# Kernel tuning notes

Measured on AMD Instinct MI355X. Metric: run time of the kernel, lower is better.

Reference implementation:

```python
import jax, jax.numpy as jnp
import numpy as np
from jax import lax

DIM = 512
HEADS = 8
B, H, W = 8, 64, 64
EPS = 1e-12  # F.normalize default eps


def pointwise(x, w):
    # 1x1 conv, no bias: [B,C,H,W] x [O,C] -> [B,O,H,W]
    return jnp.einsum('oc,bchw->bohw', w, x)


def depthwise3x3(x, dw):
    # groups=C depthwise 3x3 conv, padding=1, no bias. dw: [C,1,3,3]
    return lax.conv_general_dilated(
        x, dw, window_strides=(1, 1), padding=((1, 1), (1, 1)),
        feature_group_count=x.shape[1],
        dimension_numbers=('NCHW', 'OIHW', 'NCHW'))


def setup_inputs() -> dict:
    key = jax.random.key(0)
    ks = jax.random.split(key, 8)
    s = 1.0 / np.sqrt(DIM)
    return {
        'x': jax.random.normal(ks[0], (B, DIM, H, W), jnp.float32),
        'w_q': jax.random.normal(ks[1], (DIM, DIM), jnp.float32) * s,
        'w_k': jax.random.normal(ks[2], (DIM, DIM), jnp.float32) * s,
        'w_v': jax.random.normal(ks[3], (DIM, DIM), jnp.float32) * s,
        'dw_q': jax.random.normal(ks[4], (DIM, 1, 3, 3), jnp.float32) * (1.0 / 3.0),
        'dw_k': jax.random.normal(ks[5], (DIM, 1, 3, 3), jnp.float32) * (1.0 / 3.0),
        'dw_v': jax.random.normal(ks[6], (DIM, 1, 3, 3), jnp.float32) * (1.0 / 3.0),
        'w_proj': jax.random.normal(ks[7], (DIM, DIM), jnp.float32) * s,
        'temperature': jnp.ones((HEADS, 1, 1), jnp.float32),
    }


def reference(x, w_q, w_k, w_v, dw_q, dw_k, dw_v, w_proj, temperature):
    b, c, h, w = x.shape
    d = c // HEADS
    hw = h * w

    q = depthwise3x3(pointwise(x, w_q), dw_q)
    k = depthwise3x3(pointwise(x, w_k), dw_k)
    v = depthwise3x3(pointwise(x, w_v), dw_v)

    # b (h d) x y -> b h d (x y)
    q = q.reshape(b, HEADS, d, hw)
    k = k.reshape(b, HEADS, d, hw)
    v = v.reshape(b, HEADS, d, hw)

    # L2-normalize over spatial axis (F.normalize, eps=1e-12)
    q = q / jnp.maximum(jnp.linalg.norm(q, axis=-1, keepdims=True), EPS)
    k = k / jnp.maximum(jnp.linalg.norm(k, axis=-1, keepdims=True), EPS)

    # channel attention: [b,h,d,d]
    attn = jnp.einsum('bhdn,bhen->bhde', q, k) * temperature
    attn = jax.nn.softmax(attn, axis=-1)
    out = jnp.einsum('bhde,bhen->bhdn', attn, v)  # [b,h,d,hw]

    out = out.reshape(b, c, h, w)
    return pointwise(out, w_proj)
```

## Files before the change

### kernel.cpp

```cpp
#include <hip/hip_runtime.h>
#include <hip/hip_bf16.h>
#include <stdint.h>

#define DEV __device__ __forceinline__

typedef __attribute__((ext_vector_type(8))) short   s16x8;
typedef __attribute__((ext_vector_type(8))) __bf16  bf16x8;
typedef __attribute__((ext_vector_type(4))) float   f32x4;

static constexpr int BATCH = 8;
static constexpr int DIM   = 512;
static constexpr int HEADS = 8;
static constexpr int HD    = 64;
static constexpr int HW    = 4096;
static constexpr int CQKV  = 1536;
static constexpr int NSPLIT = 8;

DEV void gload16(const void* g, void* l) {
  __builtin_amdgcn_global_load_lds(
      (const __attribute__((address_space(1))) void*)g,
      (__attribute__((address_space(3))) void*)l,
      16, 0, 0);
}

DEV f32x4 mfma16x32(s16x8 a, s16x8 b, f32x4 c) {
  return __builtin_amdgcn_mfma_f32_16x16x32_bf16(
      __builtin_bit_cast(bf16x8, a), __builtin_bit_cast(bf16x8, b), c, 0, 0, 0);
}

DEV float b2f(short x) {
  unsigned u = (unsigned)(unsigned short)x << 16;
  return __uint_as_float(u);
}
DEV short f2b(float f) { return __builtin_bit_cast(short, __float2bfloat16(f)); }

__global__ __launch_bounds__(256) void prep_weights(
    const float* __restrict__ wq, const float* __restrict__ wk,
    const float* __restrict__ wv, const float* __restrict__ wp,
    __hip_bfloat16* __restrict__ wqkv, __hip_bfloat16* __restrict__ wpb)
{
  int i = blockIdx.x * 256 + threadIdx.x;
  if (i < CQKV * DIM) {
    int r = i / DIM;
    const float* src = (r < 512) ? wq : (r < 1024) ? wk : wv;
    wqkv[i] = __float2bfloat16(src[(r & 511) * DIM + (i % DIM)]);
  } else {
    int j = i - CQKV * DIM;
    wpb[j] = __float2bfloat16(wp[j]);
  }
}

__global__ __launch_bounds__(256) void transpose_x(
    const float* __restrict__ x, __hip_bfloat16* __restrict__ XT)
{
  __shared__ float tile[64 * 65];
  const int n0 = blockIdx.x * 64, c0 = blockIdx.y * 64, b = blockIdx.z;
  const int t = threadIdx.x;
#pragma unroll
  for (int i = 0; i < 16; ++i) {
    int f = i * 256 + t; int ci = f >> 6, nj = f & 63;
    tile[ci * 65 + nj] = x[((long)b * DIM + c0 + ci) * HW + n0 + nj];
  }
  __syncthreads();
#pragma unroll
  for (int i = 0; i < 16; ++i) {
    int f = i * 256 + t; int ni = f >> 6, cj = f & 63;
    XT[((long)b * HW + n0 + ni) * DIM + c0 + cj] = __float2bfloat16(tile[cj * 65 + ni]);
  }
}

__global__ __launch_bounds__(256) void gemm_bt(
    const __hip_bfloat16* __restrict__ A,
    const __hip_bfloat16* __restrict__ Bt,
    __hip_bfloat16* __restrict__ Cout,
    int M, int N, int K, long bt_bstride, long c_bstride)
{
  __shared__ __hip_bfloat16 lds[16896];
  const int t = threadIdx.x, w = t >> 6, l = t & 63;
  const int m0 = blockIdx.y * 128, n0 = blockIdx.x * 128, b = blockIdx.z;
  const int wr = w >> 1, wc = w & 1;
  const __hip_bfloat16* Bb = Bt + (long)b * bt_bstride;
  __hip_bfloat16* ldsA = lds;
  __hip_bfloat16* ldsB = lds + 8192;

  f32x4 acc[4][4] = {};

  for (int k0 = 0; k0 < K; k0 += 64) {
#pragma unroll
    for (int i = 0; i < 4; ++i) {
      int r = w * 32 + i * 8 + (l >> 3);
      int c = (l & 7) ^ (r & 7);
      gload16(A  + (long)(m0 + r) * K + k0 + c * 8, &ldsA[w * 2048 + i * 512]);
      gload16(Bb + (long)(n0 + r) * K + k0 + c * 8, &ldsB[w * 2048 + i * 512]);
    }
    __syncthreads();
#pragma unroll
    for (int kk = 0; kk < 64; kk += 32) {
      s16x8 af[4], bfr[4];
#pragma unroll
      for (int mi = 0; mi < 4; ++mi) {
        int ar = wr * 64 + mi * 16 + (l & 15);
        int col = (kk + (l >> 4) * 8) ^ ((ar & 7) << 3);
        af[mi] = *(const s16x8*)&ldsA[ar * 64 + col];
      }
#pragma unroll
      for (int ni = 0; ni < 4; ++ni) {
        int br = wc * 64 + ni * 16 + (l & 15);
        int col = (kk + (l >> 4) * 8) ^ ((br & 7) << 3);
        bfr[ni] = *(const s16x8*)&ldsB[br * 64 + col];
      }
#pragma unroll
      for (int mi = 0; mi < 4; ++mi)
#pragma unroll
        for (int ni = 0; ni < 4; ++ni)
          acc[mi][ni] = mfma16x32(af[mi], bfr[ni], acc[mi][ni]);
    }
    __syncthreads();
  }

#pragma unroll
  for (int mi = 0; mi < 4; ++mi)
#pragma unroll
    for (int ni = 0; ni < 4; ++ni)
#pragma unroll
      for (int j = 0; j < 4; ++j) {
        int r = wr * 64 + mi * 16 + (l >> 4) * 4 + j;
        int c = wc * 64 + ni * 16 + (l & 15);
        lds[r * 132 + c] = __float2bfloat16(acc[mi][ni][j]);
      }
  __syncthreads();
  __hip_bfloat16* crow = Cout + (long)b * c_bstride + (long)m0 * N + n0;
#pragma unroll
  for (int q = 0; q < 8; ++q) {
    int chunk = q * 256 + t;
    int r = chunk >> 4, c = (chunk & 15) * 8;
    s16x8 v = *(const s16x8*)&lds[r * 132 + c];
    *(s16x8*)&crow[(long)r * N + c] = v;
  }
}

template <bool OUT_BF16>
__global__ __launch_bounds__(512, 2) void gemm_bt8(
    const __hip_bfloat16* __restrict__ A,
    const __hip_bfloat16* __restrict__ Bt,
    void* __restrict__ Cout,
    int M, int N, int K, long bt_bstride, long c_bstride)
{
  __shared__ __hip_bfloat16 lds[65536];
  const int t = threadIdx.x, w = t >> 6, l = t & 63;
  const int wm = w >> 2, wn = w & 3;
  const int m0 = blockIdx.y * 256, n0 = blockIdx.x * 256, b = blockIdx.z;
  const __hip_bfloat16* Bb = Bt + (long)b * bt_bstride;

  const int rl = t >> 3;
  const int ch = ((t & 7) ^ (rl & 7)) * 8;
  const int fr = l & 15, fk = (l >> 4) * 8;
  const int fswz = (l & 7) << 3;

  auto stageA = [&](int p, int h, int u) {
    const __hip_bfloat16* src = A + (long)(m0 + h * 64 + rl) * K + u * 64 + ch;
    __hip_bfloat16* dst = lds + p * 16384 + h * 8192 + w * 512;
    gload16(src, dst);
    gload16(src + 128l * K, dst + 4096);
  };
  auto stageB = [&](int p, int hb, int u) {
    const __hip_bfloat16* src = Bb + (long)(n0 + hb * 128 + rl) * K + u * 64 + ch;
    __hip_bfloat16* dst = lds + 32768 + p * 16384 + hb * 8192 + w * 512;
    gload16(src, dst);
    gload16(src + 64l * K, dst + 4096);
  };

  f32x4 acc[8][4] = {};
  const int NT = K >> 6;

  stageB(0, 0, 0); stageB(0, 1, 0); stageA(0, 0, 0); stageA(0, 1, 0);
  stageB(1, 0, 1); stageB(1, 1, 1); stageA(1, 0, 1);
  asm volatile("s_waitcnt vmcnt(6)" ::: "memory");
  __builtin_amdgcn_s_barrier();

  for (int u = 0; u < NT; ++u) {
    const int p = u & 1;
    const __hip_bfloat16* lA = lds + p * 16384 + wm * 4096;
    const __hip_bfloat16* lB = lds + 32768 + p * 16384 + (wn >> 1) * 8192
                             + (wn & 1) * 4096;
    s16x8 bfr[2][4];
#pragma unroll
    for (int q = 0; q < 4; ++q) {
      s16x8 afr[2][2];
#pragma unroll
      for (int kk = 0; kk < 2; ++kk)
#pragma unroll
        for (int mi = 0; mi < 2; ++mi)
          afr[kk][mi] = *(const s16x8*)&lA[(q >> 1) * 8192
              + ((q & 1) * 32 + mi * 16 + fr) * 64 + ((kk * 32 + fk) ^ fswz)];
      if (q == 0) {
#pragma unroll
        for (int kk = 0; kk < 2; ++kk)
#pragma unroll
          for (int ni = 0; ni < 4; ++ni)
            bfr[kk][ni] = *(const s16x8*)&lB[(ni * 16 + fr) * 64
                + ((kk * 32 + fk) ^ fswz)];
      }
      if (q == 0)      { if (u + 1 < NT) stageA(p ^ 1, 1, u + 1); }
      else if (q == 1) { if (u + 2 < NT) stageB(p, 0, u + 2); }
      else if (q == 2) { if (u + 2 < NT) stageB(p, 1, u + 2); }
      else {
        if (u + 2 < NT) stageA(p, 0, u + 2);
        if (u == NT - 2) asm volatile("s_waitcnt vmcnt(0)" ::: "memory");
        else             asm volatile("s_waitcnt vmcnt(6)" ::: "memory");
      }
      __builtin_amdgcn_s_barrier();
      asm volatile("s_waitcnt lgkmcnt(0)" ::: "memory");
      __builtin_amdgcn_sched_barrier(0);
      __builtin_amdgcn_s_setprio(1);
#pragma unroll
      for (int kk = 0; kk < 2; ++kk)
#pragma unroll
        for (int mi = 0; mi < 2; ++mi)
#pragma unroll
          for (int ni = 0; ni < 4; ++ni)
            acc[q * 2 + mi][ni] = mfma16x32(afr[kk][mi], bfr[kk][ni],
                                            acc[q * 2 + mi][ni]);
      __builtin_amdgcn_s_setprio(0);
      __builtin_amdgcn_s_barrier();
    }
  }

  const int row0 = m0 + wm * 128, col0 = n0 + wn * 64;
#pragma unroll
  for (int mi = 0; mi < 8; ++mi)
#pragma unroll
    for (int ni = 0; ni < 4; ++ni)
#pragma unroll
      for (int j = 0; j < 4; ++j) {
        long rr = row0 + mi * 16 + (l >> 4) * 4 + j;
        long cc = col0 + ni * 16 + fr;
        float v = acc[mi][ni][j];
        if (OUT_BF16)
          ((__hip_bfloat16*)Cout)[(long)b * c_bstride + rr * N + cc] = __float2bfloat16(v);
        else
          ((float*)Cout)[(long)b * c_bstride + rr * N + cc] = v;
      }
}

__global__ __launch_bounds__(256) void dwconv(
    __hip_bfloat16* __restrict__ P,
    const float* __restrict__ dwq, const float* __restrict__ dwk,
    const float* __restrict__ dwv, float* __restrict__ rnorm)
{
  __shared__ float pl[66 * 67];
  __shared__ float red4[4];
  const int c = blockIdx.x, b = blockIdx.y, t = threadIdx.x;
  const int w = t >> 6, l = t & 63;

  if (t < 66) { pl[t] = 0.f; pl[65 * 67 + t] = 0.f; }
  if (t >= 128 && t < 192) { pl[(t - 127) * 67] = 0.f; }
  if (t >= 192)            { pl[(t - 191) * 67 + 65] = 0.f; }

  const long base = ((long)b * CQKV + c) * HW;
  const int y = t >> 2, x0 = (t & 3) * 16;
  s16x8 v0 = *(const s16x8*)&P[base + t * 16];
  s16x8 v1 = *(const s16x8*)&P[base + t * 16 + 8];
#pragma unroll
  for (int j = 0; j < 8; ++j) {
    pl[(y + 1) * 67 + x0 + 1 + j] = b2f(v0[j]);
    pl[(y + 1) * 67 + x0 + 9 + j] = b2f(v1[j]);
  }
  __syncthreads();

  const int qkv = c >> 9, cc = c & 511;
  const float* dw = ((qkv == 0) ? dwq : (qkv == 1) ? dwk : dwv) + (long)cc * 9;
  const float w0 = dw[0], w1 = dw[1], w2 = dw[2], w3 = dw[3], w4 = dw[4],
              w5 = dw[5], w6 = dw[6], w7 = dw[7], w8 = dw[8];

  const float* r0 = &pl[y * 67 + x0];
  float outv[16];
  float ss = 0.f;
#pragma unroll
  for (int j = 0; j < 16; ++j) {
    float s = w0 * r0[j]       + w1 * r0[j + 1]   + w2 * r0[j + 2]
            + w3 * r0[j + 67]  + w4 * r0[j + 68]  + w5 * r0[j + 69]
            + w6 * r0[j + 134] + w7 * r0[j + 135] + w8 * r0[j + 136];
    outv[j] = s;
    ss += s * s;
  }
  s16x8 o0, o1;
#pragma unroll
  for (int j = 0; j < 8; ++j) { o0[j] = f2b(outv[j]); o1[j] = f2b(outv[j + 8]); }
  *(s16x8*)&P[base + t * 16]     = o0;
  *(s16x8*)&P[base + t * 16 + 8] = o1;

  if (qkv < 2) {
#pragma unroll
    for (int off = 32; off; off >>= 1) ss += __shfl_down(ss, off);
    if (l == 0) red4[w] = ss;
    __syncthreads();
    if (t == 0)
      rnorm[(long)b * 1024 + qkv * 512 + cc] =
          1.f / fmaxf(sqrtf(red4[0] + red4[1] + red4[2] + red4[3]), 1e-12f);
  }
}

__global__ __launch_bounds__(256) void transpose_v(
    const __hip_bfloat16* __restrict__ P, __hip_bfloat16* __restrict__ VT)
{
  __shared__ __hip_bfloat16 tile[64 * 65];
  const int n0 = blockIdx.x * 64, h = blockIdx.y, b = blockIdx.z;
  const int t = threadIdx.x;
#pragma unroll
  for (int i = 0; i < 16; ++i) {
    int f = i * 256 + t; int ei = f >> 6, nj = f & 63;
    tile[ei * 65 + nj] = P[((long)b * CQKV + 1024 + h * HD + ei) * HW + n0 + nj];
  }
  __syncthreads();
#pragma unroll
  for (int i = 0; i < 16; ++i) {
    int f = i * 256 + t; int ni = f >> 6, ej = f & 63;
    VT[(((long)b * HEADS + h) * HW + n0 + ni) * HD + ej] = tile[ej * 65 + ni];
  }
}

__global__ __launch_bounds__(256) void attn_partial(__hip_bfloat16* __restrict__ P)
{
  __shared__ __hip_bfloat16 ldsQ[64 * 128];
  __shared__ __hip_bfloat16 ldsK[64 * 128];
  const int t = threadIdx.x, w = t >> 6, l = t & 63;
  const int sp = blockIdx.x, h = blockIdx.y, b = blockIdx.z;
  const int wr = w >> 1, wc = w & 1;

  const long qbase = ((long)b * CQKV + h * HD) * HW;
  const long kbase = ((long)b * CQKV + 512 + h * HD) * HW;

  f32x4 acc[2][2] = {};

  const int kend = sp * 512 + 512;
  for (int k0 = sp * 512; k0 < kend; k0 += 128) {
#pragma unroll
    for (int i = 0; i < 4; ++i) {
      int r = w * 16 + i * 4 + (l >> 4);
      int c = (l & 15) ^ (r & 7);
      gload16(P + qbase + (long)r * HW + k0 + c * 8, &ldsQ[w * 2048 + i * 512]);
      gload16(P + kbase + (long)r * HW + k0 + c * 8, &ldsK[w * 2048 + i * 512]);
    }
    __syncthreads();
#pragma unroll
    for (int kk = 0; kk < 128; kk += 32) {
      s16x8 af[2], bfr[2];
#pragma unroll
      for (int mi = 0; mi < 2; ++mi) {
        int ar = wr * 32 + mi * 16 + (l & 15);
        int col = (kk + (l >> 4) * 8) ^ ((ar & 7) << 3);
        af[mi] = *(const s16x8*)&ldsQ[ar * 128 + col];
      }
#pragma unroll
      for (int ni = 0; ni < 2; ++ni) {
        int br = wc * 32 + ni * 16 + (l & 15);
        int col = (kk + (l >> 4) * 8) ^ ((br & 7) << 3);
        bfr[ni] = *(const s16x8*)&ldsK[br * 128 + col];
      }
#pragma unroll
      for (int mi = 0; mi < 2; ++mi)
#pragma unroll
        for (int ni = 0; ni < 2; ++ni)
          acc[mi][ni] = mfma16x32(af[mi], bfr[ni], acc[mi][ni]);
    }
    __syncthreads();
  }

  float* part = (float*)((char*)P + (long)b * (CQKV * HW * 2) + (1024l * HW * 2))
              + ((long)h * NSPLIT + sp) * 4096;
#pragma unroll
  for (int mi = 0; mi < 2; ++mi)
#pragma unroll
    for (int ni = 0; ni < 2; ++ni)
#pragma unroll
      for (int j = 0; j < 4; ++j) {
        int row = wr * 32 + mi * 16 + (l >> 4) * 4 + j;
        int col = wc * 32 + ni * 16 + (l & 15);
        part[row * 64 + col] = acc[mi][ni][j];
      }
}

__global__ __launch_bounds__(256) void attn_softmax(
    const __hip_bfloat16* __restrict__ P, const float* __restrict__ rnorm,
    const float* __restrict__ temp, __hip_bfloat16* __restrict__ attnb)
{
  __shared__ float S[64 * 65];
  const int t = threadIdx.x, h = blockIdx.x, b = blockIdx.y;
  const float* part = (const float*)((const char*)P + (long)b * (CQKV * HW * 2)
                                     + (1024l * HW * 2))
                    + (long)h * NSPLIT * 4096;
  const float tm = temp[h];

  for (int i = t; i < 4096; i += 256) {
    float s = 0.f;
#pragma unroll
    for (int p = 0; p < NSPLIT; ++p) s += part[p * 4096 + i];
    int r = i >> 6, c = i & 63;
    float rq = rnorm[(long)b * 1024 + h * HD + r];
    float rk = rnorm[(long)b * 1024 + 512 + h * HD + c];
    S[r * 65 + c] = s * rq * rk * tm;
  }
  __syncthreads();

  if (t < 64) {
    float m = -3.4e38f;
    for (int e = 0; e < 64; ++e) m = fmaxf(m, S[t * 65 + e]);
    float sum = 0.f;
    for (int e = 0; e < 64; ++e) {
      float ev = __expf(S[t * 65 + e] - m);
      S[t * 65 + e] = ev;
      sum += ev;
    }
    float inv = 1.f / sum;
    for (int e = 0; e < 64; ++e)
      attnb[(((long)b * HEADS + h) * 64 + t) * 64 + e] =
          __float2bfloat16(S[t * 65 + e] * inv);
  }
}

__global__ __launch_bounds__(256) void attn_apply_v(
    const __hip_bfloat16* __restrict__ VT, const __hip_bfloat16* __restrict__ attnb,
    __hip_bfloat16* __restrict__ OT)
{
  __shared__ __hip_bfloat16 ldsV[128 * 64];
  __shared__ __hip_bfloat16 ldsAt[64 * 64];
  const int t = threadIdx.x, w = t >> 6, l = t & 63;
  const int bh = blockIdx.y, b = bh >> 3, h = bh & 7;
  const int n0 = blockIdx.x * 128;

#pragma unroll
  for (int i = 0; i < 4; ++i) {
    int r = w * 32 + i * 8 + (l >> 3);
    int c = (l & 7) ^ (r & 7);
    gload16(VT + ((long)bh * HW + n0 + r) * HD + c * 8, &ldsV[w * 2048 + i * 512]);
  }
#pragma unroll
  for (int i = 0; i < 2; ++i) {
    int r = w * 16 + i * 8 + (l >> 3);
    int c = (l & 7) ^ (r & 7);
    gload16(attnb + ((long)bh * 64 + r) * 64 + c * 8, &ldsAt[w * 1024 + i * 512]);
  }
  __syncthreads();

  f32x4 acc[2][4] = {};
#pragma unroll
  for (int kk = 0; kk < 64; kk += 32) {
    s16x8 af[2], bfr[4];
#pragma unroll
    for (int mi = 0; mi < 2; ++mi) {
      int ar = w * 32 + mi * 16 + (l & 15);
      int col = (kk + (l >> 4) * 8) ^ ((ar & 7) << 3);
      af[mi] = *(const s16x8*)&ldsV[ar * 64 + col];
    }
#pragma unroll
    for (int ni = 0; ni < 4; ++ni) {
      int br = ni * 16 + (l & 15);
      int col = (kk + (l >> 4) * 8) ^ ((br & 7) << 3);
      bfr[ni] = *(const s16x8*)&ldsAt[br * 64 + col];
    }
#pragma unroll
    for (int mi = 0; mi < 2; ++mi)
#pragma unroll
      for (int ni = 0; ni < 4; ++ni)
        acc[mi][ni] = mfma16x32(af[mi], bfr[ni], acc[mi][ni]);
  }

#pragma unroll
  for (int mi = 0; mi < 2; ++mi)
#pragma unroll
    for (int ni = 0; ni < 4; ++ni)
#pragma unroll
      for (int j = 0; j < 4; ++j) {
        long n = n0 + w * 32 + mi * 16 + (l >> 4) * 4 + j;
        long c = h * HD + ni * 16 + (l & 15);
        OT[((long)b * HW + n) * DIM + c] = __float2bfloat16(acc[mi][ni][j]);
      }
}

extern "C" void kernel_launch(void* const* d_in, const int* in_sizes, int n_in,
                              void* d_out, int out_size, void* d_ws, size_t ws_size,
                              hipStream_t stream)
{
  const float* x    = (const float*)d_in[0];
  const float* wq   = (const float*)d_in[1];
  const float* wk   = (const float*)d_in[2];
  const float* wv   = (const float*)d_in[3];
  const float* dwq  = (const float*)d_in[4];
  const float* dwk  = (const float*)d_in[5];
  const float* dwv  = (const float*)d_in[6];
  const float* wp   = (const float*)d_in[7];
  const float* temp = (const float*)d_in[8];
  float* out = (float*)d_out;

  char* ws = (char*)d_ws;
  __hip_bfloat16* wqkv  = (__hip_bfloat16*)(ws + 0);
  __hip_bfloat16* wpb   = (__hip_bfloat16*)(ws + 1572864);
  float*          rnorm = (float*)(ws + 2097152);
  __hip_bfloat16* attnb = (__hip_bfloat16*)(ws + 2129920);
  __hip_bfloat16* XT    = (__hip_bfloat16*)(ws + (4l << 20));
  __hip_bfloat16* VT    = XT;
  __hip_bfloat16* P     = (__hip_bfloat16*)(ws + (40l << 20));
  __hip_bfloat16* OT    = P;

  prep_weights<<<4096, 256, 0, stream>>>(wq, wk, wv, wp, wqkv, wpb);
  transpose_x<<<dim3(64, 8, 8), 256, 0, stream>>>(x, XT);
  gemm_bt<<<dim3(32, 12, 8), 256, 0, stream>>>(
      wqkv, XT, P, CQKV, HW, DIM, (long)HW * DIM, (long)CQKV * HW);
  dwconv<<<dim3(1536, 8), 256, 0, stream>>>(P, dwq, dwk, dwv, rnorm);
  transpose_v<<<dim3(64, 8, 8), 256, 0, stream>>>(P, VT);
  attn_partial<<<dim3(NSPLIT, 8, 8), 256, 0, stream>>>(P);
  attn_softmax<<<dim3(8, 8), 256, 0, stream>>>(P, rnorm, temp, attnb);
  attn_apply_v<<<dim3(32, 64), 256, 0, stream>>>(VT, attnb, OT);
  gemm_bt8<false><<<dim3(16, 2, 8), 512, 0, stream>>>(
      wpb, OT, out, DIM, HW, DIM, (long)HW * DIM, (long)DIM * HW);
}
```

Before: 195.7 us.

## Fuse weight prep into x transpose and softmax into partial attention

Merges the weight bf16 conversion into the x-transpose launch as an extra z-slice, now vectorized eight elements per thread. It also folds the softmax kernel into the split-K attention-partial kernel: the last split block for each (batch, head), found with an atomic counter, reduces the partials and does the softmax. This removes two launches and their gaps, but adds a memset of the counters, threadfences and a serialized tail in one block per head.

```diff
diff --git a/kernel.cpp b/kernel.cpp
--- a/kernel.cpp
+++ b/kernel.cpp
@@ -34,28 +34,37 @@
 }
 DEV short f2b(float f) { return __builtin_bit_cast(short, __float2bfloat16(f)); }
 
-__global__ __launch_bounds__(256) void prep_weights(
+__global__ __launch_bounds__(256) void trx_prep(
+    const float* __restrict__ x, __hip_bfloat16* __restrict__ XT,
     const float* __restrict__ wq, const float* __restrict__ wk,
     const float* __restrict__ wv, const float* __restrict__ wp,
     __hip_bfloat16* __restrict__ wqkv, __hip_bfloat16* __restrict__ wpb)
 {
-  int i = blockIdx.x * 256 + threadIdx.x;
-  if (i < CQKV * DIM) {
-    int r = i / DIM;
-    const float* src = (r < 512) ? wq : (r < 1024) ? wk : wv;
-    wqkv[i] = __float2bfloat16(src[(r & 511) * DIM + (i % DIM)]);
-  } else {
-    int j = i - CQKV * DIM;
-    wpb[j] = __float2bfloat16(wp[j]);
-  }
-}
-
-__global__ __launch_bounds__(256) void transpose_x(
-    const float* __restrict__ x, __hip_bfloat16* __restrict__ XT)
-{
+  const int t = threadIdx.x;
+  if (blockIdx.z == 8) {
+    long i0 = (((long)blockIdx.y * 64 + blockIdx.x) * 256 + t) * 8;
+    const float* src;
+    __hip_bfloat16* dst;
+    long off;
+    if (i0 < (long)CQKV * DIM) {
+      int r = (int)(i0 >> 9);
+      src = (r < 512) ? wq : (r < 1024) ? wk : wv;
+      off = (long)(r & 511) * DIM + (i0 & 511);
+      dst = wqkv + i0;
+    } else {
+      long j0 = i0 - (long)CQKV * DIM;
+      src = wp; off = j0; dst = wpb + j0;
+    }
+    float4 a = *(const float4*)&src[off];
+    float4 b = *(const float4*)&src[off + 4];
+    s16x8 v;
+    v[0] = f2b(a.x); v[1] = f2b(a.y); v[2] = f2b(a.z); v[3] = f2b(a.w);
+    v[4] = f2b(b.x); v[5] = f2b(b.y); v[6] = f2b(b.z); v[7] = f2b(b.w);
+    *(s16x8*)dst = v;
+    return;
+  }
   __shared__ float tile[64 * 65];
   const int n0 = blockIdx.x * 64, c0 = blockIdx.y * 64, b = blockIdx.z;
-  const int t = threadIdx.x;
 #pragma unroll
   for (int i = 0; i < 16; ++i) {
     int f = i * 256 + t; int ci = f >> 6, nj = f & 63;
@@ -320,10 +329,14 @@
   }
 }
 
-__global__ __launch_bounds__(256) void attn_partial(__hip_bfloat16* __restrict__ P)
+__global__ __launch_bounds__(256) void attn_partial_sm(
+    __hip_bfloat16* __restrict__ P, const float* __restrict__ rnorm,
+    const float* __restrict__ temp, __hip_bfloat16* __restrict__ attnb,
+    int* __restrict__ cnt)
 {
   __shared__ __hip_bfloat16 ldsQ[64 * 128];
   __shared__ __hip_bfloat16 ldsK[64 * 128];
+  __shared__ int lastflag;
   const int t = threadIdx.x, w = t >> 6, l = t & 63;
   const int sp = blockIdx.x, h = blockIdx.y, b = blockIdx.z;
   const int wr = w >> 1, wc = w & 1;
@@ -367,8 +380,8 @@
     __syncthreads();
   }
 
-  float* part = (float*)((char*)P + (long)b * (CQKV * HW * 2) + (1024l * HW * 2))
-              + ((long)h * NSPLIT + sp) * 4096;
+  float* partbase = (float*)((char*)P + (long)b * (CQKV * HW * 2) + (1024l * HW * 2));
+  float* part = partbase + ((long)h * NSPLIT + sp) * 4096;
 #pragma unroll
   for (int mi = 0; mi < 2; ++mi)
 #pragma unroll
@@ -379,43 +392,40 @@
         int col = wc * 32 + ni * 16 + (l & 15);
         part[row * 64 + col] = acc[mi][ni][j];
       }
-}
-
-__global__ __launch_bounds__(256) void attn_softmax(
-    const __hip_bfloat16* __restrict__ P, const float* __restrict__ rnorm,
-    const float* __restrict__ temp, __hip_bfloat16* __restrict__ attnb)
-{
-  __shared__ float S[64 * 65];
-  const int t = threadIdx.x, h = blockIdx.x, b = blockIdx.y;
-  const float* part = (const float*)((const char*)P + (long)b * (CQKV * HW * 2)
-                                     + (1024l * HW * 2))
-                    + (long)h * NSPLIT * 4096;
+
+  __threadfence();
+  __syncthreads();
+  if (t == 0) lastflag = atomicAdd(&cnt[b * HEADS + h], 1);
+  __syncthreads();
+  if (lastflag != NSPLIT - 1) return;
+  __threadfence();
+
+  float* S = (float*)ldsQ;
+  const float* allpart = partbase + (long)h * NSPLIT * 4096;
   const float tm = temp[h];
-
   for (int i = t; i < 4096; i += 256) {
     float s = 0.f;
 #pragma unroll
-    for (int p = 0; p < NSPLIT; ++p) s += part[p * 4096 + i];
+    for (int p = 0; p < NSPLIT; ++p) s += allpart[p * 4096 + i];
     int r = i >> 6, c = i & 63;
     float rq = rnorm[(long)b * 1024 + h * HD + r];
     float rk = rnorm[(long)b * 1024 + 512 + h * HD + c];
-    S[r * 65 + c] = s * rq * rk * tm;
-  }
-  __syncthreads();
-
+    S[r * 66 + c] = s * rq * rk * tm;
+  }
+  __syncthreads();
   if (t < 64) {
     float m = -3.4e38f;
-    for (int e = 0; e < 64; ++e) m = fmaxf(m, S[t * 65 + e]);
+    for (int e = 0; e < 64; ++e) m = fmaxf(m, S[t * 66 + e]);
     float sum = 0.f;
     for (int e = 0; e < 64; ++e) {
-      float ev = __expf(S[t * 65 + e] - m);
-      S[t * 65 + e] = ev;
+      float ev = __expf(S[t * 66 + e] - m);
+      S[t * 66 + e] = ev;
       sum += ev;
     }
     float inv = 1.f / sum;
     for (int e = 0; e < 64; ++e)
       attnb[(((long)b * HEADS + h) * 64 + t) * 64 + e] =
-          __float2bfloat16(S[t * 65 + e] * inv);
+          __float2bfloat16(S[t * 66 + e] * inv);
   }
 }
 
@@ -498,19 +508,19 @@
   __hip_bfloat16* wpb   = (__hip_bfloat16*)(ws + 1572864);
   float*          rnorm = (float*)(ws + 2097152);
   __hip_bfloat16* attnb = (__hip_bfloat16*)(ws + 2129920);
+  int*            cnt   = (int*)(ws + 3145728);
   __hip_bfloat16* XT    = (__hip_bfloat16*)(ws + (4l << 20));
   __hip_bfloat16* VT    = XT;
   __hip_bfloat16* P     = (__hip_bfloat16*)(ws + (40l << 20));
   __hip_bfloat16* OT    = P;
 
-  prep_weights<<<4096, 256, 0, stream>>>(wq, wk, wv, wp, wqkv, wpb);
-  transpose_x<<<dim3(64, 8, 8), 256, 0, stream>>>(x, XT);
+  hipMemsetAsync(cnt, 0, 256, stream);
+  trx_prep<<<dim3(64, 8, 9), 256, 0, stream>>>(x, XT, wq, wk, wv, wp, wqkv, wpb);
   gemm_bt<<<dim3(32, 12, 8), 256, 0, stream>>>(
       wqkv, XT, P, CQKV, HW, DIM, (long)HW * DIM, (long)CQKV * HW);
   dwconv<<<dim3(1536, 8), 256, 0, stream>>>(P, dwq, dwk, dwv, rnorm);
   transpose_v<<<dim3(64, 8, 8), 256, 0, stream>>>(P, VT);
-  attn_partial<<<dim3(NSPLIT, 8, 8), 256, 0, stream>>>(P);
-  attn_softmax<<<dim3(8, 8), 256, 0, stream>>>(P, rnorm, temp, attnb);
+  attn_partial_sm<<<dim3(NSPLIT, 8, 8), 256, 0, stream>>>(P, rnorm, temp, attnb, cnt);
   attn_apply_v<<<dim3(32, 64), 256, 0, stream>>>(VT, attnb, OT);
   gemm_bt8<false><<<dim3(16, 2, 8), 512, 0, stream>>>(
       wpb, OT, out, DIM, HW, DIM, (long)HW * DIM, (long)DIM * HW);
```

Result: slower. 269.0 us (median of 2 runs) (+37.5%).

## Fuse weight prep into x transpose and enlarge QKV GEMM tiles

Applied to the files above, without the earlier changes.

Merges the weight conversion kernel into the x-transpose kernel as an extra grid slice, with vectorized 8-element conversion, which removes one launch. The QKV projection GEMM moves from 128x128 tiles with 256 threads to 256x256 tiles with 512 threads, so each wave computes 8x4 MFMA fragments for more operand reuse. The LDS-staged coalesced epilogue is replaced by direct scalar bf16 global stores. That cuts LDS use and a barrier, but the output writes become poorly coalesced, and the larger tiles give fewer blocks (768) and more register pressure.

```diff
diff --git a/kernel.cpp b/kernel.cpp
--- a/kernel.cpp
+++ b/kernel.cpp
@@ -34,28 +34,37 @@
 }
 DEV short f2b(float f) { return __builtin_bit_cast(short, __float2bfloat16(f)); }
 
-__global__ __launch_bounds__(256) void prep_weights(
+__global__ __launch_bounds__(256) void trx_prep(
+    const float* __restrict__ x, __hip_bfloat16* __restrict__ XT,
     const float* __restrict__ wq, const float* __restrict__ wk,
     const float* __restrict__ wv, const float* __restrict__ wp,
     __hip_bfloat16* __restrict__ wqkv, __hip_bfloat16* __restrict__ wpb)
 {
-  int i = blockIdx.x * 256 + threadIdx.x;
-  if (i < CQKV * DIM) {
-    int r = i / DIM;
-    const float* src = (r < 512) ? wq : (r < 1024) ? wk : wv;
-    wqkv[i] = __float2bfloat16(src[(r & 511) * DIM + (i % DIM)]);
-  } else {
-    int j = i - CQKV * DIM;
-    wpb[j] = __float2bfloat16(wp[j]);
-  }
-}
-
-__global__ __launch_bounds__(256) void transpose_x(
-    const float* __restrict__ x, __hip_bfloat16* __restrict__ XT)
-{
+  const int t = threadIdx.x;
+  if (blockIdx.z == 8) {
+    long i0 = (((long)blockIdx.y * 64 + blockIdx.x) * 256 + t) * 8;
+    const float* src;
+    __hip_bfloat16* dst;
+    long off;
+    if (i0 < (long)CQKV * DIM) {
+      int r = (int)(i0 >> 9);
+      src = (r < 512) ? wq : (r < 1024) ? wk : wv;
+      off = (long)(r & 511) * DIM + (i0 & 511);
+      dst = wqkv + i0;
+    } else {
+      long j0 = i0 - (long)CQKV * DIM;
+      src = wp; off = j0; dst = wpb + j0;
+    }
+    float4 a = *(const float4*)&src[off];
+    float4 b = *(const float4*)&src[off + 4];
+    s16x8 v;
+    v[0] = f2b(a.x); v[1] = f2b(a.y); v[2] = f2b(a.z); v[3] = f2b(a.w);
+    v[4] = f2b(b.x); v[5] = f2b(b.y); v[6] = f2b(b.z); v[7] = f2b(b.w);
+    *(s16x8*)dst = v;
+    return;
+  }
   __shared__ float tile[64 * 65];
   const int n0 = blockIdx.x * 64, c0 = blockIdx.y * 64, b = blockIdx.z;
-  const int t = threadIdx.x;
 #pragma unroll
   for (int i = 0; i < 16; ++i) {
     int f = i * 256 + t; int ci = f >> 6, nj = f & 63;
@@ -69,48 +78,50 @@
   }
 }
 
-__global__ __launch_bounds__(256) void gemm_bt(
+__global__ __launch_bounds__(512) void gemm_bt2(
     const __hip_bfloat16* __restrict__ A,
     const __hip_bfloat16* __restrict__ Bt,
     __hip_bfloat16* __restrict__ Cout,
     int M, int N, int K, long bt_bstride, long c_bstride)
 {
-  __shared__ __hip_bfloat16 lds[16896];
+  __shared__ __hip_bfloat16 lds[32768];
   const int t = threadIdx.x, w = t >> 6, l = t & 63;
-  const int m0 = blockIdx.y * 128, n0 = blockIdx.x * 128, b = blockIdx.z;
-  const int wr = w >> 1, wc = w & 1;
+  const int wm = w >> 2, wn = w & 3;
+  const int m0 = blockIdx.y * 256, n0 = blockIdx.x * 256, b = blockIdx.z;
   const __hip_bfloat16* Bb = Bt + (long)b * bt_bstride;
   __hip_bfloat16* ldsA = lds;
-  __hip_bfloat16* ldsB = lds + 8192;
-
-  f32x4 acc[4][4] = {};
+  __hip_bfloat16* ldsB = lds + 16384;
+
+  const int fr = l & 15, g = l >> 4;
+  f32x4 acc[8][4] = {};
 
   for (int k0 = 0; k0 < K; k0 += 64) {
 #pragma unroll
-    for (int i = 0; i < 4; ++i) {
-      int r = w * 32 + i * 8 + (l >> 3);
-      int c = (l & 7) ^ (r & 7);
-      gload16(A  + (long)(m0 + r) * K + k0 + c * 8, &ldsA[w * 2048 + i * 512]);
-      gload16(Bb + (long)(n0 + r) * K + k0 + c * 8, &ldsB[w * 2048 + i * 512]);
+    for (int q = 0; q < 4; ++q) {
+      int id = q * 512 + t;
+      int r = id >> 3;
+      int c = (id & 7) ^ (r & 7);
+      gload16(A  + (long)(m0 + r) * K + k0 + c * 8, &ldsA[id * 8]);
+      gload16(Bb + (long)(n0 + r) * K + k0 + c * 8, &ldsB[id * 8]);
     }
     __syncthreads();
 #pragma unroll
     for (int kk = 0; kk < 64; kk += 32) {
-      s16x8 af[4], bfr[4];
-#pragma unroll
-      for (int mi = 0; mi < 4; ++mi) {
-        int ar = wr * 64 + mi * 16 + (l & 15);
-        int col = (kk + (l >> 4) * 8) ^ ((ar & 7) << 3);
+      s16x8 af[8], bfr[4];
+#pragma unroll
+      for (int mi = 0; mi < 8; ++mi) {
+        int ar = wm * 128 + mi * 16 + fr;
+        int col = (kk + g * 8) ^ ((ar & 7) << 3);
         af[mi] = *(const s16x8*)&ldsA[ar * 64 + col];
       }
 #pragma unroll
       for (int ni = 0; ni < 4; ++ni) {
-        int br = wc * 64 + ni * 16 + (l & 15);
-        int col = (kk + (l >> 4) * 8) ^ ((br & 7) << 3);
+        int br = wn * 64 + ni * 16 + fr;
+        int col = (kk + g * 8) ^ ((br & 7) << 3);
         bfr[ni] = *(const s16x8*)&ldsB[br * 64 + col];
       }
 #pragma unroll
-      for (int mi = 0; mi < 4; ++mi)
+      for (int mi = 0; mi < 8; ++mi)
 #pragma unroll
         for (int ni = 0; ni < 4; ++ni)
           acc[mi][ni] = mfma16x32(af[mi], bfr[ni], acc[mi][ni]);
@@ -118,25 +129,17 @@
     __syncthreads();
   }
 
-#pragma unroll
-  for (int mi = 0; mi < 4; ++mi)
+  const int row0 = m0 + wm * 128, col0 = n0 + wn * 64;
+#pragma unroll
+  for (int mi = 0; mi < 8; ++mi)
 #pragma unroll
     for (int ni = 0; ni < 4; ++ni)
 #pragma unroll
       for (int j = 0; j < 4; ++j) {
-        int r = wr * 64 + mi * 16 + (l >> 4) * 4 + j;
-        int c = wc * 64 + ni * 16 + (l & 15);
-        lds[r * 132 + c] = __float2bfloat16(acc[mi][ni][j]);
-      }
-  __syncthreads();
-  __hip_bfloat16* crow = Cout + (long)b * c_bstride + (long)m0 * N + n0;
-#pragma unroll
-  for (int q = 0; q < 8; ++q) {
-    int chunk = q * 256 + t;
-    int r = chunk >> 4, c = (chunk & 15) * 8;
-    s16x8 v = *(const s16x8*)&lds[r * 132 + c];
-    *(s16x8*)&crow[(long)r * N + c] = v;
-  }
+        long rr = row0 + mi * 16 + (l >> 4) * 4 + j;
+        long cc = col0 + ni * 16 + fr;
+        Cout[(long)b * c_bstride + rr * N + cc] = __float2bfloat16(acc[mi][ni][j]);
+      }
 }
 
 template <bool OUT_BF16>
@@ -503,9 +506,8 @@
   __hip_bfloat16* P     = (__hip_bfloat16*)(ws + (40l << 20));
   __hip_bfloat16* OT    = P;
 
-  prep_weights<<<4096, 256, 0, stream>>>(wq, wk, wv, wp, wqkv, wpb);
-  transpose_x<<<dim3(64, 8, 8), 256, 0, stream>>>(x, XT);
-  gemm_bt<<<dim3(32, 12, 8), 256, 0, stream>>>(
+  trx_prep<<<dim3(64, 8, 9), 256, 0, stream>>>(x, XT, wq, wk, wv, wp, wqkv, wpb);
+  gemm_bt2<<<dim3(16, 6, 8), 512, 0, stream>>>(
       wqkv, XT, P, CQKV, HW, DIM, (long)HW * DIM, (long)CQKV * HW);
   dwconv<<<dim3(1536, 8), 256, 0, stream>>>(P, dwq, dwk, dwv, rnorm);
   transpose_v<<<dim3(64, 8, 8), 256, 0, stream>>>(P, VT);
```

Result: no change. 192.7 us (-1.5%).
